# Performance work log

Hardware: AMD Instinct MI355X
Metric: run time of the kernel (lower is better)

The kernel has to match this reference:

```python
import jax, jax.numpy as jnp
import numpy as np

B, T, D, H = 8, 256, 1024, 512
NUM_SPANS = T * (T + 1) // 2          # triangular span enumeration
K = int(2.0 * T)                      # pruning_ratio * num_tokens
NUM_GOLD = 10
NEG = -1e20                           # allennlp replace_masked_values fill

# static triangular (start, end) index tables: for start in range(T): for end in range(start, T)
_starts = np.repeat(np.arange(T), np.arange(T, 0, -1))
_ends = np.concatenate([np.arange(s, T) for s in range(T)])
START_IDX = jnp.asarray(_starts, dtype=jnp.int32)
END_IDX = jnp.asarray(_ends, dtype=jnp.int32)


def setup_inputs() -> dict:
    key = jax.random.key(0)
    ks = jax.random.split(key, 8)
    inputs = jax.random.normal(ks[0], (B, T, D), dtype=jnp.float32)
    input_mask = jnp.ones((B, T), dtype=jnp.int32)
    # gold spans with start <= end, all in range (sorted along last dim)
    answer_spans = jnp.sort(jax.random.randint(ks[1], (B, NUM_GOLD, 2), 0, T), axis=-1)
    sD = 1.0 / np.sqrt(D)
    sH = 1.0 / np.sqrt(H)
    W_start = jax.random.uniform(ks[2], (D, H), jnp.float32, -sD, sD)
    b_start = jax.random.uniform(ks[3], (H,), jnp.float32, -sD, sD)
    W_end = jax.random.uniform(ks[4], (D, H), jnp.float32, -sD, sD)
    b_end = jax.random.uniform(ks[5], (H,), jnp.float32, -sD, sD)
    w_score = jax.random.uniform(ks[6], (H, 1), jnp.float32, -sH, sH)
    b_score = jax.random.uniform(ks[7], (1,), jnp.float32, -sH, sH)
    return {"inputs": inputs, "input_mask": input_mask, "answer_spans": answer_spans,
            "W_start": W_start, "b_start": b_start, "W_end": W_end, "b_end": b_end,
            "w_score": w_score, "b_score": b_score}


def reference(inputs, input_mask, answer_spans, W_start, b_start, W_end, b_end, w_score, b_score):
    # SpanRepAssembly: project starts/ends, pairwise-sum over triangular spans
    hs = inputs @ W_start + b_start                        # [B,T,H]
    he = inputs @ W_end + b_end                            # [B,T,H]
    span_hidden = hs[:, START_IDX, :] + he[:, END_IDX, :]  # [B,S,H]
    m = input_mask.astype(bool)
    span_mask = m[:, START_IDX] & m[:, END_IDX]            # [B,S]

    # span scorer: ReLU -> Linear(H,1)
    scores = jax.nn.relu(span_hidden) @ w_score + b_score  # [B,S,1]
    scores = jnp.where(span_mask[..., None], scores, NEG)

    # Pruner: top-k by score, indices sorted ascending, gather
    _, top_idx = jax.lax.top_k(scores[..., 0], K)          # [B,K]
    top_idx = jnp.sort(top_idx, axis=1)
    top_logits = jnp.take_along_axis(scores, top_idx[..., None], axis=1)       # [B,K,1]
    top_mask = jnp.take_along_axis(span_mask, top_idx, axis=1)[..., None].astype(jnp.float32)
    top_probs = jax.nn.sigmoid(top_logits) * top_mask

    # gold prediction map (union policy): labels[b, tri_index(span)] = 1
    s0 = answer_spans[..., 0].astype(jnp.int32)
    e0 = answer_spans[..., 1].astype(jnp.int32)
    gmask = (s0 >= 0)
    arg_idx = (2 * s0 * T - s0 * s0 + s0) // 2 + (e0 - s0)
    arg_idx = jnp.where(gmask, arg_idx, 0)
    labels = jnp.zeros((B, NUM_SPANS), jnp.float32)
    labels = labels.at[jnp.arange(B)[:, None], arg_idx].max(gmask.astype(jnp.float32))
    pred = jnp.take_along_axis(labels[..., None], top_idx[..., None], axis=1)  # [B,K,1]

    # BCE-with-logits, weight=top_mask, reduction='sum' (stable form)
    l = top_logits
    bce = jnp.maximum(l, 0.0) - l * pred + jnp.log1p(jnp.exp(-jnp.abs(l)))
    loss = jnp.sum(top_mask * bce)
    return top_probs, loss
```

## Files before the change

### kernel.cpp

```cpp
#include <hip/hip_runtime.h>
#include <hip/hip_bf16.h>
#include <math.h>

#define BB 8
#define TT 256
#define DD 1024
#define HH 512
#define NSPANS 32896
#define KK 512
#define NEGV -1e20f
#define NCH 32
#define CHSZ 1028
#define NT32 36

typedef __attribute__((ext_vector_type(8))) short bf16x8;
typedef __attribute__((ext_vector_type(4))) float f32x4;

__device__ inline unsigned short f2bf(float f) {
    unsigned u = __float_as_uint(f);
    return (unsigned short)((u + 0x7FFFu + ((u >> 16) & 1u)) >> 16);
}
__device__ inline float bf2f(unsigned short u) {
    return __uint_as_float(((unsigned)u) << 16);
}
__device__ inline void split3(float v, unsigned short& a, unsigned short& b,
                              unsigned short& c) {
    a = f2bf(v);           float r  = v - bf2f(a);
    b = f2bf(r);           float r2 = r - bf2f(b);
    c = f2bf(r2);
}

__global__ __launch_bounds__(256) void prep(
    const float* __restrict__ X,
    const float* __restrict__ Ws, const float* __restrict__ We,
    unsigned short* __restrict__ x0, unsigned short* __restrict__ x1,
    unsigned short* __restrict__ x2, unsigned short* __restrict__ wt,
    unsigned* __restrict__ zp)
{
    const int blk = blockIdx.x;
    const int tid = threadIdx.x;

    if (blk < 2048) {
        const int i4 = blk * 256 + tid;
        const float4 v = ((const float4*)X)[i4];
        const float vv[4] = {v.x, v.y, v.z, v.w};
        ushort4 h0, h1, h2;
        unsigned short* p0 = (unsigned short*)&h0;
        unsigned short* p1 = (unsigned short*)&h1;
        unsigned short* p2 = (unsigned short*)&h2;
        #pragma unroll
        for (int j = 0; j < 4; ++j) split3(vv[j], p0[j], p1[j], p2[j]);
        ((ushort4*)x0)[i4] = h0;
        ((ushort4*)x1)[i4] = h1;
        ((ushort4*)x2)[i4] = h2;
    } else if (blk < 6144) {
        const int idx = (blk - 2048) * 256 + tid;
        const int z = idx >> 19;
        const int p = idx & 524287;
        const int h = p >> 10, d = p & 1023;
        const float v = (z ? We : Ws)[d * HH + h];
        unsigned short a, b, c;
        split3(v, a, b, c);
        unsigned short* base = wt + (size_t)z * 3 * 524288;
        base[0 * 524288 + p] = a;
        base[1 * 524288 + p] = b;
        base[2 * 524288 + p] = c;
    } else {
        const int i = (blk - 6144) * 256 + tid;
        for (int k = i; k < 32776; k += 32 * 256) zp[k] = 0u;
    }
}

__global__ __launch_bounds__(256) void gemm_mfma(
    const unsigned short* __restrict__ xs,
    const unsigned short* __restrict__ wt,
    const float* __restrict__ bs, const float* __restrict__ be,
    float* __restrict__ hs, float* __restrict__ he)
{
    const int bid = blockIdx.x;
    const int lg  = ((bid & 7) << 6) + (bid >> 3);
    const int z   = lg >> 8;
    const int my  = (lg & 255) >> 3, nx = lg & 7;
    const int m0 = my * 64, n0 = nx * 64;

    const unsigned short* __restrict__ W = wt + (size_t)z * 3 * 524288;
    const float* __restrict__ bias = z ? be : bs;
    float* __restrict__ Y = z ? he : hs;

    __shared__ __align__(16) unsigned short la[3][64][72];
    __shared__ __align__(16) unsigned short lb[3][64][72];

    const int tid = threadIdx.x;
    const int wave = tid >> 6, lane = tid & 63;
    const int wm = (wave >> 1) * 32, wn = (wave & 1) * 32;

    f32x4 acc[2][2];
    #pragma unroll
    for (int i = 0; i < 2; ++i)
        #pragma unroll
        for (int j = 0; j < 2; ++j) acc[i][j] = (f32x4){0.f, 0.f, 0.f, 0.f};

    const int rA = lane & 15;
    const int kq = lane >> 4;

    for (int kt = 0; kt < 16; ++kt) {
        const int k0 = kt * 64;
        __syncthreads();
        #pragma unroll
        for (int sp = 0; sp < 3; ++sp) {
            #pragma unroll
            for (int it = 0; it < 2; ++it) {
                const int idx = it * 256 + tid;
                const int row = idx >> 3, c8 = idx & 7;
                *(int4*)&la[sp][row][c8 * 8] =
                    *(const int4*)&xs[(size_t)sp * 2097152 + (m0 + row) * 1024 + k0 + c8 * 8];
                *(int4*)&lb[sp][row][c8 * 8] =
                    *(const int4*)&W[(size_t)sp * 524288 + (n0 + row) * 1024 + k0 + c8 * 8];
            }
        }
        __syncthreads();

        #pragma unroll
        for (int s = 0; s < 2; ++s) {
            const int kl = s * 32 + kq * 8;
            bf16x8 af[3][2], bg[3][2];
            #pragma unroll
            for (int sp = 0; sp < 3; ++sp) {
                #pragma unroll
                for (int f = 0; f < 2; ++f) {
                    af[sp][f] = *(const bf16x8*)&la[sp][wm + f * 16 + rA][kl];
                    bg[sp][f] = *(const bf16x8*)&lb[sp][wn + f * 16 + rA][kl];
                }
            }
            #pragma unroll
            for (int fm = 0; fm < 2; ++fm)
                #pragma unroll
                for (int fn = 0; fn < 2; ++fn) {
                    acc[fm][fn] = __builtin_amdgcn_mfma_f32_16x16x32_bf16(
                        af[0][fm], bg[0][fn], acc[fm][fn], 0, 0, 0);
                    acc[fm][fn] = __builtin_amdgcn_mfma_f32_16x16x32_bf16(
                        af[0][fm], bg[1][fn], acc[fm][fn], 0, 0, 0);
                    acc[fm][fn] = __builtin_amdgcn_mfma_f32_16x16x32_bf16(
                        af[1][fm], bg[0][fn], acc[fm][fn], 0, 0, 0);
                    acc[fm][fn] = __builtin_amdgcn_mfma_f32_16x16x32_bf16(
                        af[1][fm], bg[1][fn], acc[fm][fn], 0, 0, 0);
                    acc[fm][fn] = __builtin_amdgcn_mfma_f32_16x16x32_bf16(
                        af[0][fm], bg[2][fn], acc[fm][fn], 0, 0, 0);
                    acc[fm][fn] = __builtin_amdgcn_mfma_f32_16x16x32_bf16(
                        af[2][fm], bg[0][fn], acc[fm][fn], 0, 0, 0);
                }
        }
    }

    const int col = lane & 15, rq = lane >> 4;
    #pragma unroll
    for (int fm = 0; fm < 2; ++fm)
        #pragma unroll
        for (int fn = 0; fn < 2; ++fn) {
            const int nn = n0 + wn + fn * 16 + col;
            const float bv = bias[nn];
            #pragma unroll
            for (int r = 0; r < 4; ++r) {
                const int mm = m0 + wm + fm * 16 + rq * 4 + r;
                Y[mm * HH + nn] = acc[fm][fn][r] + bv;
            }
        }
}

__device__ inline unsigned f2key(float f) {
    unsigned u = __float_as_uint(f);
    return u ^ ((u & 0x80000000u) ? 0xFFFFFFFFu : 0x80000000u);
}

__global__ __launch_bounds__(256) void span_scores(
    const float* __restrict__ hs, const float* __restrict__ he,
    const float* __restrict__ w_score, const float* __restrict__ b_score,
    const int* __restrict__ input_mask, float* __restrict__ scores,
    unsigned* __restrict__ hist12)
{
    const int bx = blockIdx.x;
    const int b = bx / NT32;
    int tI = bx - b * NT32;
    int i = 0, cum = 0;
    while (tI >= cum + (8 - i)) { cum += 8 - i; ++i; }
    const int j = i + (tI - cum);
    const int s0 = i * 32, e0 = j * 32;

    __shared__ __align__(16) float shs[32][132];
    __shared__ __align__(16) float she[32][132];
    __shared__ __align__(16) float swc[128];
    __shared__ unsigned lh[2048];

    const int tid = threadIdx.x;
    const float4* hs4 = (const float4*)hs;
    const float4* he4 = (const float4*)he;

    for (int idx = tid; idx < 2048; idx += 256) lh[idx] = 0;

    const int ii = tid >> 4, jj = tid & 15;

    float4 acc[2][2];
    #pragma unroll
    for (int p = 0; p < 2; ++p)
        #pragma unroll
        for (int q = 0; q < 2; ++q) acc[p][q] = make_float4(0.f, 0.f, 0.f, 0.f);

    for (int ck = 0; ck < 4; ++ck) {
        const int kc = ck * 128;
        __syncthreads();
        #pragma unroll
        for (int l = 0; l < 4; ++l) {
            const int idx = l * 256 + tid;
            const int row = idx >> 5, c4 = idx & 31;
            *(float4*)&shs[row][c4 * 4] =
                hs4[((b*TT + s0 + row) * HH + kc) / 4 + c4];
            *(float4*)&she[row][c4 * 4] =
                he4[((b*TT + e0 + row) * HH + kc) / 4 + c4];
        }
        if (tid < 32) *(float4*)&swc[tid * 4] =
            ((const float4*)w_score)[kc / 4 + tid];
        __syncthreads();

        #pragma unroll 4
        for (int c4 = 0; c4 < 32; ++c4) {
            const float4 w  = *(const float4*)&swc[c4 * 4];
            const float4 a0 = *(const float4*)&shs[ii][c4 * 4];
            const float4 a1 = *(const float4*)&shs[ii + 16][c4 * 4];
            const float4 v0 = *(const float4*)&she[jj][c4 * 4];
            const float4 v1 = *(const float4*)&she[jj + 16][c4 * 4];
            #pragma unroll
            for (int p = 0; p < 2; ++p) {
                const float4 a = p ? a1 : a0;
                #pragma unroll
                for (int q = 0; q < 2; ++q) {
                    const float4 v = q ? v1 : v0;
                    acc[p][q].x += fmaxf(a.x + v.x, 0.f) * w.x;
                    acc[p][q].y += fmaxf(a.y + v.y, 0.f) * w.y;
                    acc[p][q].z += fmaxf(a.z + v.z, 0.f) * w.z;
                    acc[p][q].w += fmaxf(a.w + v.w, 0.f) * w.w;
                }
            }
        }
    }

    const float bsc = b_score[0];
    #pragma unroll
    for (int p = 0; p < 2; ++p) {
        const int s = s0 + ii + p * 16;
        #pragma unroll
        for (int q = 0; q < 2; ++q) {
            const int e = e0 + jj + q * 16;
            if (e >= s) {
                const float4 a4 = acc[p][q];
                float scv = (a4.x + a4.y) + (a4.z + a4.w) + bsc;
                if (!(input_mask[b*TT + s] && input_mask[b*TT + e])) scv = NEGV;
                scores[b*NSPANS + s*TT - (s*(s-1))/2 + (e - s)] = scv;
                const unsigned bin = f2key(scv) >> 20;
                atomicAdd(&lh[bin >> 1], 1u << ((bin & 1u) * 16));
            }
        }
    }
    __syncthreads();

    for (int idx = tid; idx < 2048; idx += 256) {
        const unsigned w = lh[idx];
        const unsigned lo = w & 0xFFFFu, hi = w >> 16;
        if (lo) atomicAdd(&hist12[b*4096 + 2*idx],     lo);
        if (hi) atomicAdd(&hist12[b*4096 + 2*idx + 1], hi);
    }
}

__global__ __launch_bounds__(256) void findcompact(
    const float* __restrict__ scores, const unsigned* __restrict__ hist12,
    unsigned* __restrict__ thrInfo,
    unsigned* __restrict__ cand, unsigned* __restrict__ candCnt)
{
    const int b = blockIdx.x >> 5, ch = blockIdx.x & 31;
    const unsigned* h = hist12 + b * 4096;
    const int tid = threadIdx.x;
    const int lane = tid & 63, wave = tid >> 6;

    const int topbin = 4095 - tid * 16;
    unsigned psum = 0;
    #pragma unroll
    for (int j = 0; j < 16; ++j) psum += h[topbin - j];

    unsigned inc = psum;
    #pragma unroll
    for (int off = 1; off < 64; off <<= 1) {
        unsigned v = __shfl_up(inc, off);
        if (lane >= off) inc += v;
    }
    __shared__ unsigned wsum4[4], wpre4[4];
    __shared__ unsigned shp[2];
    if (lane == 63) wsum4[wave] = inc;
    __syncthreads();
    if (tid == 0) { unsigned c = 0; for (int w = 0; w < 4; ++w) { wpre4[w] = c; c += wsum4[w]; } }
    __syncthreads();

    const unsigned before = wpre4[wave] + inc - psum;
    if (before < KK && before + psum >= KK) {
        unsigned cum = before;
        int bin = topbin;
        #pragma unroll
        for (int j = 0; j < 16; ++j) {
            const unsigned c = h[topbin - j];
            if (cum + c >= KK) { bin = topbin - j; break; }
            cum += c;
        }
        shp[0] = (unsigned)bin;
        shp[1] = KK - cum;
        thrInfo[b*4 + 0] = (unsigned)bin;
        thrInfo[b*4 + 1] = KK - cum;
    }
    __syncthreads();
    const unsigned p12 = shp[0];

    const float* sc = scores + b * NSPANS;
    const int base = ch * CHSZ;
    for (int i = base + tid; i < base + CHSZ; i += 256) {
        const unsigned key = f2key(sc[i]);
        if ((key >> 20) == p12) {
            const unsigned pos = atomicAdd(&candCnt[b], 1u);
            cand[b*NSPANS + pos] = key & 0xFFFFFu;
        }
    }
}

__global__ __launch_bounds__(1024) void refine(
    const unsigned* __restrict__ cand, const unsigned* __restrict__ candCnt,
    const float* __restrict__ scores,
    unsigned* __restrict__ thrInfo, unsigned* __restrict__ chunkBase)
{
    const int b = blockIdx.x;
    const unsigned* cd = cand + b*NSPANS;
    const unsigned n = candCnt[b];
    const unsigned remaining = thrInfo[b*4 + 1];
    const int tid = threadIdx.x;
    const int lane = tid & 63, wave = tid >> 6;

    __shared__ unsigned hist[1024];
    __shared__ unsigned wsum[16], wpre[16];
    __shared__ unsigned sh[2], shT[2];

    hist[tid] = 0;
    __syncthreads();
    for (unsigned i = tid; i < n; i += 1024) atomicAdd(&hist[(cd[i] >> 10) & 1023u], 1u);
    __syncthreads();
    {
        const unsigned psum = hist[1023 - tid];
        unsigned inc = psum;
        #pragma unroll
        for (int off = 1; off < 64; off <<= 1) {
            unsigned v = __shfl_up(inc, off);
            if (lane >= off) inc += v;
        }
        if (lane == 63) wsum[wave] = inc;
        __syncthreads();
        if (tid == 0) { unsigned c = 0; for (int w = 0; w < 16; ++w) { wpre[w] = c; c += wsum[w]; } }
        __syncthreads();
        const unsigned before = wpre[wave] + inc - psum;
        if (before < remaining && before + psum >= remaining && psum > 0) {
            sh[0] = 1023u - (unsigned)tid;
            sh[1] = remaining - before;
        }
        __syncthreads();
    }
    const unsigned b1 = sh[0], rem1 = sh[1];
    __syncthreads();

    hist[tid] = 0;
    __syncthreads();
    for (unsigned i = tid; i < n; i += 1024) {
        const unsigned v = cd[i];
        if (((v >> 10) & 1023u) == b1) atomicAdd(&hist[v & 1023u], 1u);
    }
    __syncthreads();
    {
        const unsigned psum = hist[1023 - tid];
        unsigned inc = psum;
        #pragma unroll
        for (int off = 1; off < 64; off <<= 1) {
            unsigned v = __shfl_up(inc, off);
            if (lane >= off) inc += v;
        }
        if (lane == 63) wsum[wave] = inc;
        __syncthreads();
        if (tid == 0) { unsigned c = 0; for (int w = 0; w < 16; ++w) { wpre[w] = c; c += wsum[w]; } }
        __syncthreads();
        const unsigned before = wpre[wave] + inc - psum;
        if (before < rem1 && before + psum >= rem1 && psum > 0) {
            const unsigned thrv = (thrInfo[b*4 + 0] << 20) | (b1 << 10) | (1023u - (unsigned)tid);
            thrInfo[b*4 + 2] = thrv;
            thrInfo[b*4 + 3] = rem1 - before;
            shT[0] = thrv;
            shT[1] = rem1 - before;
        }
    }
    __syncthreads();
    const unsigned thr = shT[0], ties = shT[1];

    __shared__ unsigned cg[NCH], ce[NCH];
    const float* sc = scores + b*NSPANS;
    #pragma unroll
    for (int q = 0; q < 2; ++q) {
        const int ch = wave*2 + q;
        const int base = ch*CHSZ, end = base + CHSZ;
        unsigned g = 0, e = 0;
        for (int i = base + lane; i < end; i += 64) {
            const unsigned key = f2key(sc[i]);
            g += (key > thr); e += (key == thr);
        }
        #pragma unroll
        for (int off = 32; off; off >>= 1) { g += __shfl_down(g, off); e += __shfl_down(e, off); }
        if (lane == 0) { cg[ch] = g; ce[ch] = e; }
    }
    __syncthreads();

    if (tid == 0) {
        unsigned out = 0, eqp = 0;
        for (int c = 0; c < NCH; ++c) {
            chunkBase[(b*NCH + c)*2 + 0] = out;
            chunkBase[(b*NCH + c)*2 + 1] = eqp;
            const unsigned room = (eqp >= ties) ? 0u : (ties - eqp);
            const unsigned taken = (ce[c] < room) ? ce[c] : room;
            out += cg[c] + taken;
            eqp += ce[c];
        }
    }
}

__global__ __launch_bounds__(256) void scatter(
    const float* __restrict__ scores, const unsigned* __restrict__ thrInfo,
    const unsigned* __restrict__ chunkBase, int* __restrict__ top_idx)
{
    const int b = blockIdx.x >> 5, ch = blockIdx.x & 31;
    const float* sc = scores + b*NSPANS;
    const unsigned thr = thrInfo[b*4 + 2], ties = thrInfo[b*4 + 3];
    unsigned outPos = chunkBase[(b*NCH + ch)*2 + 0];
    unsigned eqPos  = chunkBase[(b*NCH + ch)*2 + 1];

    const int tid = threadIdx.x, wave = tid >> 6, lane = tid & 63;
    const unsigned long long lmask = (1ull << lane) - 1ull;
    __shared__ unsigned wS[4], wE[4];

    const int base = ch*CHSZ;
    for (int seg = base; seg < base + CHSZ; seg += 256) {
        const int i = seg + tid;
        const bool valid = (i < base + CHSZ);
        const unsigned key = valid ? f2key(sc[i]) : 0u;
        const bool g  = valid && key > thr;
        const bool eq = valid && key == thr;

        const unsigned long long meq = __ballot(eq);
        if (lane == 0) wE[wave] = (unsigned)__popcll(meq);
        __syncthreads();

        unsigned eqPre = eqPos;
        for (int w = 0; w < wave; ++w) eqPre += wE[w];
        const unsigned myEqRank = eqPre + (unsigned)__popcll(meq & lmask);
        const bool sel = g || (eq && myEqRank < ties);

        const unsigned long long msel = __ballot(sel);
        if (lane == 0) wS[wave] = (unsigned)__popcll(msel);
        __syncthreads();

        unsigned selPre = outPos;
        for (int w = 0; w < wave; ++w) selPre += wS[w];
        if (sel) top_idx[b*KK + selPre + (unsigned)__popcll(msel & lmask)] = i;

        unsigned totS = 0, totE = 0;
        #pragma unroll
        for (int w = 0; w < 4; ++w) { totS += wS[w]; totE += wE[w]; }
        __syncthreads();
        outPos += totS; eqPos += totE;
    }
}

__global__ __launch_bounds__(1024) void finalize(
    const float* __restrict__ scores, const int* __restrict__ top_idx,
    const int* __restrict__ answer_spans, float* __restrict__ out)
{
    __shared__ int gold[BB*10];
    __shared__ float part[16];
    const int tid = threadIdx.x;

    if (tid < BB*10) {
        const int s0 = answer_spans[tid*2];
        const int e0 = answer_spans[tid*2 + 1];
        gold[tid] = (s0 >= 0) ? ((2*s0*TT - s0*s0 + s0)/2 + (e0 - s0)) : -1;
    }
    __syncthreads();

    float lsum = 0.f;
    for (int t = tid; t < BB*KK; t += 1024) {
        const int b = t >> 9;
        const int idx = top_idx[t];
        const float l = scores[b*NSPANS + idx];
        float prob = 0.f;
        if (l > -1e19f) {
            prob = 1.f / (1.f + expf(-l));
            float pred = 0.f;
            #pragma unroll
            for (int g = 0; g < 10; ++g)
                if (gold[b*10 + g] == idx) pred = 1.f;
            lsum += fmaxf(l, 0.f) - l*pred + log1pf(expf(-fabsf(l)));
        }
        out[t] = prob;
    }

    #pragma unroll
    for (int off = 32; off; off >>= 1) lsum += __shfl_down(lsum, off);
    const int wave = tid >> 6, lane = tid & 63;
    if (lane == 0) part[wave] = lsum;
    __syncthreads();
    if (tid == 0) {
        float ssum = 0.f;
        for (int w = 0; w < 16; ++w) ssum += part[w];
        out[BB*KK] = ssum;
    }
}

extern "C" void kernel_launch(void* const* d_in, const int* in_sizes, int n_in,
                              void* d_out, int out_size, void* d_ws, size_t ws_size,
                              hipStream_t stream)
{
    const float* inputs       = (const float*)d_in[0];
    const int*   input_mask   = (const int*)  d_in[1];
    const int*   answer_spans = (const int*)  d_in[2];
    const float* W_start      = (const float*)d_in[3];
    const float* b_start      = (const float*)d_in[4];
    const float* W_end        = (const float*)d_in[5];
    const float* b_end        = (const float*)d_in[6];
    const float* w_score      = (const float*)d_in[7];
    const float* b_score      = (const float*)d_in[8];
    float* out = (float*)d_out;
    unsigned* ws = (unsigned*)d_ws;

    float*    hs       = (float*)(ws);
    float*    he       = (float*)(ws + 1048576);
    float*    scores   = (float*)(ws + 2097152);
    int*      top_idx  = (int*)  (ws + 2360320);
    unsigned* thrInfo  = ws + 2364416;
    unsigned* chunkBase= ws + 2364448;
    unsigned* hist12   = ws + 2364960;
    unsigned* candCnt  = ws + 2397728;
    unsigned short* xs = (unsigned short*)(ws + 2397736);
    unsigned short* wt = (unsigned short*)(ws + 5543464);
    unsigned* cand     = (unsigned*)hs;

    prep<<<6176, 256, 0, stream>>>(inputs, W_start, W_end,
                                   xs, xs + 2097152, xs + 4194304, wt, hist12);

    gemm_mfma<<<512, 256, 0, stream>>>(xs, wt, b_start, b_end, hs, he);

    span_scores<<<BB*NT32, 256, 0, stream>>>(hs, he, w_score, b_score, input_mask,
                                             scores, hist12);

    findcompact<<<BB*NCH, 256, 0, stream>>>(scores, hist12, thrInfo, cand, candCnt);
    refine     <<<BB, 1024, 0, stream>>>(cand, candCnt, scores, thrInfo, chunkBase);
    scatter    <<<BB*NCH, 256, 0, stream>>>(scores, thrInfo, chunkBase, top_idx);

    finalize<<<1, 1024, 0, stream>>>(scores, top_idx, answer_spans, out);
}
```

Before: 114.8 us.

## Fuse finalize into scatter, tile weight transpose, shrink span-score tiles

Replaces the strided per-element weight transpose in prep with a shared-memory tiled transpose using vector stores. Halves the span_scores tile to 16x32 with 128-thread blocks for more blocks and less diagonal waste. Removes the single-block finalize kernel by computing probabilities and loss inside scatter, with a last-block ticket reduction of per-chunk losses. This adds atomic/fence logic and changes the loss summation order.

Measured after the change: 115.2 us. Within noise of the previous version (+0.4%).

```diff
diff --git a/kernel.cpp b/kernel.cpp
--- a/kernel.cpp
+++ b/kernel.cpp
@@ -11,7 +11,7 @@
 #define NEGV -1e20f
 #define NCH 32
 #define CHSZ 1028
-#define NT32 36
+#define NT16 72
 
 typedef __attribute__((ext_vector_type(8))) short bf16x8;
 typedef __attribute__((ext_vector_type(4))) float f32x4;
@@ -53,21 +53,42 @@
         ((ushort4*)x0)[i4] = h0;
         ((ushort4*)x1)[i4] = h1;
         ((ushort4*)x2)[i4] = h2;
-    } else if (blk < 6144) {
-        const int idx = (blk - 2048) * 256 + tid;
-        const int z = idx >> 19;
-        const int p = idx & 524287;
-        const int h = p >> 10, d = p & 1023;
-        const float v = (z ? We : Ws)[d * HH + h];
-        unsigned short a, b, c;
-        split3(v, a, b, c);
-        unsigned short* base = wt + (size_t)z * 3 * 524288;
-        base[0 * 524288 + p] = a;
-        base[1 * 524288 + p] = b;
-        base[2 * 524288 + p] = c;
+    } else if (blk < 3072) {
+        __shared__ float lt[32][33];
+        const int blk2 = blk - 2048;
+        const int z   = blk2 >> 9;
+        const int rem = blk2 & 511;
+        const int k0  = (rem >> 4) * 32;
+        const int h0  = (rem & 15) * 32;
+
+        const float* Wz = z ? We : Ws;
+        {
+            const int row = tid >> 3, c4 = tid & 7;
+            const float4 v = *(const float4*)&Wz[(k0 + row) * HH + h0 + c4 * 4];
+            lt[row][c4*4 + 0] = v.x;
+            lt[row][c4*4 + 1] = v.y;
+            lt[row][c4*4 + 2] = v.z;
+            lt[row][c4*4 + 3] = v.w;
+        }
+        __syncthreads();
+        {
+            const int n = h0 + (tid >> 3), kq = tid & 7;
+            ushort4 o0, o1, o2;
+            unsigned short* q0 = (unsigned short*)&o0;
+            unsigned short* q1 = (unsigned short*)&o1;
+            unsigned short* q2 = (unsigned short*)&o2;
+            #pragma unroll
+            for (int u = 0; u < 4; ++u)
+                split3(lt[kq*4 + u][tid >> 3], q0[u], q1[u], q2[u]);
+            unsigned short* base = wt + (size_t)z * 3 * 524288;
+            const int off = n * 1024 + k0 + kq * 4;
+            *(ushort4*)&base[0 * 524288 + off] = o0;
+            *(ushort4*)&base[1 * 524288 + off] = o1;
+            *(ushort4*)&base[2 * 524288 + off] = o2;
+        }
     } else {
-        const int i = (blk - 6144) * 256 + tid;
-        for (int k = i; k < 32776; k += 32 * 256) zp[k] = 0u;
+        const int i = (blk - 3072) * 256 + tid;
+        for (int k = i; k < 32777; k += 32 * 256) zp[k] = 0u;
     }
 }
 
@@ -172,21 +193,21 @@
     return u ^ ((u & 0x80000000u) ? 0xFFFFFFFFu : 0x80000000u);
 }
 
-__global__ __launch_bounds__(256) void span_scores(
+__global__ __launch_bounds__(128) void span_scores(
     const float* __restrict__ hs, const float* __restrict__ he,
     const float* __restrict__ w_score, const float* __restrict__ b_score,
     const int* __restrict__ input_mask, float* __restrict__ scores,
     unsigned* __restrict__ hist12)
 {
     const int bx = blockIdx.x;
-    const int b = bx / NT32;
-    int tI = bx - b * NT32;
-    int i = 0, cum = 0;
-    while (tI >= cum + (8 - i)) { cum += 8 - i; ++i; }
-    const int j = i + (tI - cum);
-    const int s0 = i * 32, e0 = j * 32;
-
-    __shared__ __align__(16) float shs[32][132];
+    const int b = bx / NT16;
+    int tI = bx - b * NT16;
+    int i = 0, cnt = 8;
+    while (tI >= cnt) { tI -= cnt; ++i; cnt = 8 - (i >> 1); }
+    const int j = (i >> 1) + tI;
+    const int s0 = i * 16, e0 = j * 32;
+
+    __shared__ __align__(16) float shs[16][132];
     __shared__ __align__(16) float she[32][132];
     __shared__ __align__(16) float swc[128];
     __shared__ unsigned lh[2048];
@@ -195,7 +216,7 @@
     const float4* hs4 = (const float4*)hs;
     const float4* he4 = (const float4*)he;
 
-    for (int idx = tid; idx < 2048; idx += 256) lh[idx] = 0;
+    for (int idx = tid; idx < 2048; idx += 128) lh[idx] = 0;
 
     const int ii = tid >> 4, jj = tid & 15;
 
@@ -209,13 +230,16 @@
         const int kc = ck * 128;
         __syncthreads();
         #pragma unroll
-        for (int l = 0; l < 4; ++l) {
-            const int idx = l * 256 + tid;
+        for (int l = 0; l < 12; ++l) {
+            const int idx = l * 128 + tid;
             const int row = idx >> 5, c4 = idx & 31;
-            *(float4*)&shs[row][c4 * 4] =
-                hs4[((b*TT + s0 + row) * HH + kc) / 4 + c4];
-            *(float4*)&she[row][c4 * 4] =
-                he4[((b*TT + e0 + row) * HH + kc) / 4 + c4];
+            if (row < 16) {
+                *(float4*)&shs[row][c4 * 4] =
+                    hs4[((b*TT + s0 + row) * HH + kc) / 4 + c4];
+            } else {
+                *(float4*)&she[row - 16][c4 * 4] =
+                    he4[((b*TT + e0 + row - 16) * HH + kc) / 4 + c4];
+            }
         }
         if (tid < 32) *(float4*)&swc[tid * 4] =
             ((const float4*)w_score)[kc / 4 + tid];
@@ -225,7 +249,7 @@
         for (int c4 = 0; c4 < 32; ++c4) {
             const float4 w  = *(const float4*)&swc[c4 * 4];
             const float4 a0 = *(const float4*)&shs[ii][c4 * 4];
-            const float4 a1 = *(const float4*)&shs[ii + 16][c4 * 4];
+            const float4 a1 = *(const float4*)&shs[ii + 8][c4 * 4];
             const float4 v0 = *(const float4*)&she[jj][c4 * 4];
             const float4 v1 = *(const float4*)&she[jj + 16][c4 * 4];
             #pragma unroll
@@ -246,7 +270,7 @@
     const float bsc = b_score[0];
     #pragma unroll
     for (int p = 0; p < 2; ++p) {
-        const int s = s0 + ii + p * 16;
+        const int s = s0 + ii + p * 8;
         #pragma unroll
         for (int q = 0; q < 2; ++q) {
             const int e = e0 + jj + q * 16;
@@ -262,7 +286,7 @@
     }
     __syncthreads();
 
-    for (int idx = tid; idx < 2048; idx += 256) {
+    for (int idx = tid; idx < 2048; idx += 128) {
         const unsigned w = lh[idx];
         const unsigned lo = w & 0xFFFFu, hi = w >> 16;
         if (lo) atomicAdd(&hist12[b*4096 + 2*idx],     lo);
@@ -430,9 +454,11 @@
     }
 }
 
-__global__ __launch_bounds__(256) void scatter(
+__global__ __launch_bounds__(256) void scatter_final(
     const float* __restrict__ scores, const unsigned* __restrict__ thrInfo,
-    const unsigned* __restrict__ chunkBase, int* __restrict__ top_idx)
+    const unsigned* __restrict__ chunkBase, const int* __restrict__ answer_spans,
+    float* __restrict__ chunkLoss, unsigned* __restrict__ ticket,
+    float* __restrict__ out)
 {
     const int b = blockIdx.x >> 5, ch = blockIdx.x & 31;
     const float* sc = scores + b*NSPANS;
@@ -443,12 +469,24 @@
     const int tid = threadIdx.x, wave = tid >> 6, lane = tid & 63;
     const unsigned long long lmask = (1ull << lane) - 1ull;
     __shared__ unsigned wS[4], wE[4];
-
+    __shared__ int gold[10];
+    __shared__ float wLoss[4];
+    __shared__ unsigned lastFlag;
+
+    if (tid < 10) {
+        const int s0 = answer_spans[b*20 + tid*2];
+        const int e0 = answer_spans[b*20 + tid*2 + 1];
+        gold[tid] = (s0 >= 0) ? ((2*s0*TT - s0*s0 + s0)/2 + (e0 - s0)) : -1;
+    }
+    __syncthreads();
+
+    float lsum = 0.f;
     const int base = ch*CHSZ;
     for (int seg = base; seg < base + CHSZ; seg += 256) {
         const int i = seg + tid;
         const bool valid = (i < base + CHSZ);
-        const unsigned key = valid ? f2key(sc[i]) : 0u;
+        const float v = valid ? sc[i] : 0.f;
+        const unsigned key = valid ? f2key(v) : 0u;
         const bool g  = valid && key > thr;
         const bool eq = valid && key == thr;
 
@@ -467,7 +505,19 @@
 
         unsigned selPre = outPos;
         for (int w = 0; w < wave; ++w) selPre += wS[w];
-        if (sel) top_idx[b*KK + selPre + (unsigned)__popcll(msel & lmask)] = i;
+        if (sel) {
+            const unsigned pos = b*KK + selPre + (unsigned)__popcll(msel & lmask);
+            float prob = 0.f;
+            if (v > -1e19f) {
+                prob = 1.f / (1.f + expf(-v));
+                float pred = 0.f;
+                #pragma unroll
+                for (int gq = 0; gq < 10; ++gq)
+                    if (gold[gq] == i) pred = 1.f;
+                lsum += fmaxf(v, 0.f) - v*pred + log1pf(expf(-fabsf(v)));
+            }
+            out[pos] = prob;
+        }
 
         unsigned totS = 0, totE = 0;
         #pragma unroll
@@ -475,49 +525,27 @@
         __syncthreads();
         outPos += totS; eqPos += totE;
     }
-}
-
-__global__ __launch_bounds__(1024) void finalize(
-    const float* __restrict__ scores, const int* __restrict__ top_idx,
-    const int* __restrict__ answer_spans, float* __restrict__ out)
-{
-    __shared__ int gold[BB*10];
-    __shared__ float part[16];
-    const int tid = threadIdx.x;
-
-    if (tid < BB*10) {
-        const int s0 = answer_spans[tid*2];
-        const int e0 = answer_spans[tid*2 + 1];
-        gold[tid] = (s0 >= 0) ? ((2*s0*TT - s0*s0 + s0)/2 + (e0 - s0)) : -1;
-    }
-    __syncthreads();
-
-    float lsum = 0.f;
-    for (int t = tid; t < BB*KK; t += 1024) {
-        const int b = t >> 9;
-        const int idx = top_idx[t];
-        const float l = scores[b*NSPANS + idx];
-        float prob = 0.f;
-        if (l > -1e19f) {
-            prob = 1.f / (1.f + expf(-l));
-            float pred = 0.f;
-            #pragma unroll
-            for (int g = 0; g < 10; ++g)
-                if (gold[b*10 + g] == idx) pred = 1.f;
-            lsum += fmaxf(l, 0.f) - l*pred + log1pf(expf(-fabsf(l)));
-        }
-        out[t] = prob;
-    }
 
     #pragma unroll
     for (int off = 32; off; off >>= 1) lsum += __shfl_down(lsum, off);
-    const int wave = tid >> 6, lane = tid & 63;
-    if (lane == 0) part[wave] = lsum;
+    if (lane == 0) wLoss[wave] = lsum;
     __syncthreads();
     if (tid == 0) {
-        float ssum = 0.f;
-        for (int w = 0; w < 16; ++w) ssum += part[w];
-        out[BB*KK] = ssum;
+        chunkLoss[b*NCH + ch] = (wLoss[0] + wLoss[1]) + (wLoss[2] + wLoss[3]);
+        __threadfence();
+        lastFlag = atomicAdd(ticket, 1u);
+    }
+    __syncthreads();
+
+    if (lastFlag == BB*NCH - 1) {
+        __threadfence();
+        float cl = atomicAdd(&chunkLoss[tid], 0.f);
+        #pragma unroll
+        for (int off = 32; off; off >>= 1) cl += __shfl_down(cl, off);
+        if (lane == 0) wLoss[wave] = cl;
+        __syncthreads();
+        if (tid == 0)
+            out[BB*KK] = (wLoss[0] + wLoss[1]) + (wLoss[2] + wLoss[3]);
     }
 }
 
@@ -540,26 +568,26 @@
     float*    hs       = (float*)(ws);
     float*    he       = (float*)(ws + 1048576);
     float*    scores   = (float*)(ws + 2097152);
-    int*      top_idx  = (int*)  (ws + 2360320);
     unsigned* thrInfo  = ws + 2364416;
     unsigned* chunkBase= ws + 2364448;
     unsigned* hist12   = ws + 2364960;
     unsigned* candCnt  = ws + 2397728;
-    unsigned short* xs = (unsigned short*)(ws + 2397736);
-    unsigned short* wt = (unsigned short*)(ws + 5543464);
+    unsigned* ticket   = ws + 2397736;
+    unsigned short* xs = (unsigned short*)(ws + 2397740);
+    unsigned short* wt = (unsigned short*)(ws + 5543468);
+    float*    chunkLoss= (float*)(ws + 8689196);
     unsigned* cand     = (unsigned*)hs;
 
-    prep<<<6176, 256, 0, stream>>>(inputs, W_start, W_end,
+    prep<<<3104, 256, 0, stream>>>(inputs, W_start, W_end,
                                    xs, xs + 2097152, xs + 4194304, wt, hist12);
 
     gemm_mfma<<<512, 256, 0, stream>>>(xs, wt, b_start, b_end, hs, he);
 
-    span_scores<<<BB*NT32, 256, 0, stream>>>(hs, he, w_score, b_score, input_mask,
+    span_scores<<<BB*NT16, 128, 0, stream>>>(hs, he, w_score, b_score, input_mask,
                                              scores, hist12);
 
-    findcompact<<<BB*NCH, 256, 0, stream>>>(scores, hist12, thrInfo, cand, candCnt);
-    refine     <<<BB, 1024, 0, stream>>>(cand, candCnt, scores, thrInfo, chunkBase);
-    scatter    <<<BB*NCH, 256, 0, stream>>>(scores, thrInfo, chunkBase, top_idx);
-
-    finalize<<<1, 1024, 0, stream>>>(scores, top_idx, answer_spans, out);
-}
+    findcompact  <<<BB*NCH, 256, 0, stream>>>(scores, hist12, thrInfo, cand, candCnt);
+    refine       <<<BB, 1024, 0, stream>>>(cand, candCnt, scores, thrInfo, chunkBase);
+    scatter_final<<<BB*NCH, 256, 0, stream>>>(scores, thrInfo, chunkBase,
+                                              answer_spans, chunkLoss, ticket, out);
+}
```
